# Performance work log

Measured on AMD Instinct MI355X. Metric: run time of the kernel, lower is better.

## Reference

```python
import jax, jax.numpy as jnp
import numpy as np

VOLUME_SIZE = 48  # max_disp / down = 192 / 4


def setup_inputs() -> dict:
    key = jax.random.key(0)
    k1, k2 = jax.random.split(key)
    b, c, h, w = 8, 128, 128, 240
    left_feature = jax.random.normal(k1, (b, c, h, w), dtype=jnp.float32)
    right_feature = jax.random.normal(k2, (b, c, h, w), dtype=jnp.float32)
    return {"left_feature": left_feature, "right_feature": right_feature}


def reference(left_feature, right_feature):
    # cost_volume[:, i, :, x] = mean_c(L[:, :, :, x] * R[:, :, :, x-i]) for x >= i, else 0
    b, c, h, w = left_feature.shape
    col = jnp.arange(w)

    def per_disp(i):
        # shift right feature right by i; zero out wrapped-around columns (< i)
        r_shift = jnp.roll(right_feature, i, axis=-1)  # [b,c,h,w]
        prod_mean = jnp.mean(left_feature * r_shift, axis=1)  # [b,h,w]
        return jnp.where(col >= i, prod_mean, 0.0)

    cv = jax.vmap(per_disp)(jnp.arange(VOLUME_SIZE))  # [V,b,h,w]
    return jnp.transpose(cv, (1, 0, 2, 3))  # [b,V,h,w]
```

## Files before the change

### kernel.cpp

```cpp
#include <hip/hip_runtime.h>

#define CV_B 8
#define CV_C 128
#define CV_H 128
#define CV_W 240
#define CV_V 48
#define LSTRIDE 136

typedef __attribute__((ext_vector_type(8))) short bf16x8;
typedef __attribute__((ext_vector_type(4))) float f32x4;

__device__ __forceinline__ unsigned int pack2_bf16(float f0, float f1) {
    unsigned int u0 = __float_as_uint(f0);
    unsigned int u1 = __float_as_uint(f1);
    u0 += 0x7fffu + ((u0 >> 16) & 1u);
    u1 += 0x7fffu + ((u1 >> 16) & 1u);
    return (u0 >> 16) | (u1 & 0xffff0000u);
}

__global__ __launch_bounds__(256, 4) void cost_volume_kernel(
        const float* __restrict__ Lf, const float* __restrict__ Rf,
        float* __restrict__ out)
{
    __shared__ __align__(16) short sL[16 * LSTRIDE];
    __shared__ __align__(16) short sR[64 * LSTRIDE];
    __shared__ float band[CV_V * 17];

    const int t   = threadIdx.x;
    const int xt  = blockIdx.x * 16;
    const int y   = blockIdx.y;
    const int b   = blockIdx.z;
    const int jt0 = xt - 48;

    const int plane = CV_H * CV_W;
    const float* Lbase = Lf + ((b * CV_C) * plane) + y * CV_W;
    const float* Rbase = Rf + ((b * CV_C) * plane) + y * CV_W;

    {
        const int xl = t & 15;
        const int c0 = (t >> 4) * 8;
        const float* p = Lbase + c0 * plane + (xt + xl);
        float v[8];
#pragma unroll
        for (int jj = 0; jj < 8; ++jj) v[jj] = p[jj * plane];
        uint4 w;
        w.x = pack2_bf16(v[0], v[1]);
        w.y = pack2_bf16(v[2], v[3]);
        w.z = pack2_bf16(v[4], v[5]);
        w.w = pack2_bf16(v[6], v[7]);
        *(uint4*)&sL[xl * LSTRIDE + c0] = w;
    }

    {
        const int jl = t & 63;
        const int cb = (t >> 6) * 32;
        const int jg = jt0 + jl;
        const bool ok = (jg >= 0);
        const float* p = Rbase + cb * plane + jg;
#pragma unroll
        for (int g = 0; g < 4; ++g) {
            float v[8];
#pragma unroll
            for (int jj = 0; jj < 8; ++jj)
                v[jj] = ok ? p[(g * 8 + jj) * plane] : 0.0f;
            uint4 w;
            w.x = pack2_bf16(v[0], v[1]);
            w.y = pack2_bf16(v[2], v[3]);
            w.z = pack2_bf16(v[4], v[5]);
            w.w = pack2_bf16(v[6], v[7]);
            *(uint4*)&sR[jl * LSTRIDE + cb + g * 8] = w;
        }
    }

    __syncthreads();

    const int lane = t & 63;
    const int wv   = t >> 6;
    const int n    = lane & 15;
    const int quad = lane >> 4;

    f32x4 acc = {0.f, 0.f, 0.f, 0.f};
#pragma unroll
    for (int ks = 0; ks < 4; ++ks) {
        const int k0 = ks * 32 + quad * 8;
        bf16x8 a  = *(const bf16x8*)&sL[n * LSTRIDE + k0];
        bf16x8 bb = *(const bf16x8*)&sR[(wv * 16 + n) * LSTRIDE + k0];
        acc = __builtin_amdgcn_mfma_f32_16x16x32_bf16(a, bb, acc, 0, 0, 0);
    }

    const int jg = jt0 + wv * 16 + n;
#pragma unroll
    for (int r = 0; r < 4; ++r) {
        const int xl = quad * 4 + r;
        const int i  = (xt + xl) - jg;
        if (i >= 0 && i < CV_V) band[i * 17 + xl] = acc[r] * (1.0f / 128.0f);
    }
    __syncthreads();

#pragma unroll
    for (int u = 0; u < 3; ++u) {
        const int idx = t + u * 256;
        const int i   = idx >> 4;
        const int xl  = idx & 15;
        out[((b * CV_V + i) * CV_H + y) * CV_W + xt + xl] = band[i * 17 + xl];
    }
}

extern "C" void kernel_launch(void* const* d_in, const int* in_sizes, int n_in,
                              void* d_out, int out_size, void* d_ws, size_t ws_size,
                              hipStream_t stream)
{
    const float* Lf = (const float*)d_in[0];
    const float* Rf = (const float*)d_in[1];
    float* o = (float*)d_out;
    dim3 grid(CV_W / 16, CV_H, CV_B);
    dim3 block(256);
    hipLaunchKernelGGL(cost_volume_kernel, grid, block, 0, stream, Lf, Rf, o);
}
```

Before: 304.2 us.

## Sweep whole image row per block with ring-buffered right-feature tiles and prefetch

Each block now processes one full image row, iterating over 15 column tiles instead of one tile per block. Right-feature tiles are kept in a 5-slot shared-memory ring, so each R column is loaded from global memory once rather than roughly four times. The next tile's loads are issued before the current tile's MFMA and store phase. The grid shrinks to 1024 blocks of 256 threads, which may lower occupancy and parallelism, and it adds two barriers per tile.

```diff
diff --git a/kernel.cpp b/kernel.cpp
--- a/kernel.cpp
+++ b/kernel.cpp
@@ -5,7 +5,9 @@
 #define CV_H 128
 #define CV_W 240
 #define CV_V 48
+#define NT   15
 #define LSTRIDE 136
+#define NSLOT 5
 
 typedef __attribute__((ext_vector_type(8))) short bf16x8;
 typedef __attribute__((ext_vector_type(4))) float f32x4;
@@ -22,56 +24,42 @@
         const float* __restrict__ Lf, const float* __restrict__ Rf,
         float* __restrict__ out)
 {
-    __shared__ __align__(16) short sL[16 * LSTRIDE];
-    __shared__ __align__(16) short sR[64 * LSTRIDE];
+    __shared__ __align__(16) short sL[2][16 * LSTRIDE];
+    __shared__ __align__(16) short sR[NSLOT][16 * LSTRIDE];
     __shared__ float band[CV_V * 17];
 
-    const int t   = threadIdx.x;
-    const int xt  = blockIdx.x * 16;
-    const int y   = blockIdx.y;
-    const int b   = blockIdx.z;
-    const int jt0 = xt - 48;
+    const int t = threadIdx.x;
+    const int y = blockIdx.x;
+    const int b = blockIdx.y;
 
     const int plane = CV_H * CV_W;
-    const float* Lbase = Lf + ((b * CV_C) * plane) + y * CV_W;
-    const float* Rbase = Rf + ((b * CV_C) * plane) + y * CV_W;
+    const float* Lrow = Lf + (b * CV_C) * plane + y * CV_W;
+    const float* Rrow = Rf + (b * CV_C) * plane + y * CV_W;
+
+    const int xl = t & 15;
+    const int c0 = (t >> 4) * 8;
 
     {
-        const int xl = t & 15;
-        const int c0 = (t >> 4) * 8;
-        const float* p = Lbase + c0 * plane + (xt + xl);
-        float v[8];
+        uint4 z = {0u, 0u, 0u, 0u};
+        short* base = &sR[2][0];
+        const int n128 = (3 * 16 * LSTRIDE) / 8;
+        for (int idx = t; idx < n128; idx += 256)
+            *(uint4*)&base[idx * 8] = z;
+    }
+    {
+        const float* pL = Lrow + c0 * plane + xl;
+        const float* pR = Rrow + c0 * plane + xl;
+        float lv[8], rv[8];
 #pragma unroll
-        for (int jj = 0; jj < 8; ++jj) v[jj] = p[jj * plane];
-        uint4 w;
-        w.x = pack2_bf16(v[0], v[1]);
-        w.y = pack2_bf16(v[2], v[3]);
-        w.z = pack2_bf16(v[4], v[5]);
-        w.w = pack2_bf16(v[6], v[7]);
-        *(uint4*)&sL[xl * LSTRIDE + c0] = w;
+        for (int jj = 0; jj < 8; ++jj) { lv[jj] = pL[jj * plane]; rv[jj] = pR[jj * plane]; }
+        uint4 wl, wr;
+        wl.x = pack2_bf16(lv[0], lv[1]); wl.y = pack2_bf16(lv[2], lv[3]);
+        wl.z = pack2_bf16(lv[4], lv[5]); wl.w = pack2_bf16(lv[6], lv[7]);
+        wr.x = pack2_bf16(rv[0], rv[1]); wr.y = pack2_bf16(rv[2], rv[3]);
+        wr.z = pack2_bf16(rv[4], rv[5]); wr.w = pack2_bf16(rv[6], rv[7]);
+        *(uint4*)&sL[0][xl * LSTRIDE + c0] = wl;
+        *(uint4*)&sR[0][xl * LSTRIDE + c0] = wr;
     }
-
-    {
-        const int jl = t & 63;
-        const int cb = (t >> 6) * 32;
-        const int jg = jt0 + jl;
-        const bool ok = (jg >= 0);
-        const float* p = Rbase + cb * plane + jg;
-#pragma unroll
-        for (int g = 0; g < 4; ++g) {
-            float v[8];
-#pragma unroll
-            for (int jj = 0; jj < 8; ++jj)
-                v[jj] = ok ? p[(g * 8 + jj) * plane] : 0.0f;
-            uint4 w;
-            w.x = pack2_bf16(v[0], v[1]);
-            w.y = pack2_bf16(v[2], v[3]);
-            w.z = pack2_bf16(v[4], v[5]);
-            w.w = pack2_bf16(v[6], v[7]);
-            *(uint4*)&sR[jl * LSTRIDE + cb + g * 8] = w;
-        }
-    }
-
     __syncthreads();
 
     const int lane = t & 63;
@@ -79,30 +67,57 @@
     const int n    = lane & 15;
     const int quad = lane >> 4;
 
-    f32x4 acc = {0.f, 0.f, 0.f, 0.f};
+    for (int tt = 0; tt < NT; ++tt) {
+        float lv[8], rv[8];
+        const bool pf = (tt + 1 < NT);
+        if (pf) {
+            const int xg = 16 * (tt + 1);
+            const float* pL = Lrow + c0 * plane + xg + xl;
+            const float* pR = Rrow + c0 * plane + xg + xl;
 #pragma unroll
-    for (int ks = 0; ks < 4; ++ks) {
-        const int k0 = ks * 32 + quad * 8;
-        bf16x8 a  = *(const bf16x8*)&sL[n * LSTRIDE + k0];
-        bf16x8 bb = *(const bf16x8*)&sR[(wv * 16 + n) * LSTRIDE + k0];
-        acc = __builtin_amdgcn_mfma_f32_16x16x32_bf16(a, bb, acc, 0, 0, 0);
-    }
+            for (int jj = 0; jj < 8; ++jj) { lv[jj] = pL[jj * plane]; rv[jj] = pR[jj * plane]; }
+        }
 
-    const int jg = jt0 + wv * 16 + n;
+        const int u    = tt - 3 + wv;
+        const int slot = (u + NSLOT) % NSLOT;
+        const short* aRow = &sL[tt & 1][n * LSTRIDE];
+        const short* bRow = &sR[slot][n * LSTRIDE];
+        f32x4 acc = {0.f, 0.f, 0.f, 0.f};
 #pragma unroll
-    for (int r = 0; r < 4; ++r) {
-        const int xl = quad * 4 + r;
-        const int i  = (xt + xl) - jg;
-        if (i >= 0 && i < CV_V) band[i * 17 + xl] = acc[r] * (1.0f / 128.0f);
-    }
-    __syncthreads();
+        for (int ks = 0; ks < 4; ++ks) {
+            const int k0 = ks * 32 + quad * 8;
+            bf16x8 a  = *(const bf16x8*)&aRow[k0];
+            bf16x8 bb = *(const bf16x8*)&bRow[k0];
+            acc = __builtin_amdgcn_mfma_f32_16x16x32_bf16(a, bb, acc, 0, 0, 0);
+        }
 
 #pragma unroll
-    for (int u = 0; u < 3; ++u) {
-        const int idx = t + u * 256;
-        const int i   = idx >> 4;
-        const int xl  = idx & 15;
-        out[((b * CV_V + i) * CV_H + y) * CV_W + xt + xl] = band[i * 17 + xl];
+        for (int r = 0; r < 4; ++r) {
+            const int xloc = quad * 4 + r;
+            const int i    = 16 * (3 - wv) + xloc - n;
+            if (i >= 0 && i < CV_V) band[i * 17 + xloc] = acc[r] * (1.0f / 128.0f);
+        }
+        __syncthreads();
+
+        const int xbase = 16 * tt;
+#pragma unroll
+        for (int uu = 0; uu < 3; ++uu) {
+            const int idx = t + uu * 256;
+            const int i   = idx >> 4;
+            const int xx  = idx & 15;
+            out[((b * CV_V + i) * CV_H + y) * CV_W + xbase + xx] = band[i * 17 + xx];
+        }
+
+        if (pf) {
+            uint4 wl, wr;
+            wl.x = pack2_bf16(lv[0], lv[1]); wl.y = pack2_bf16(lv[2], lv[3]);
+            wl.z = pack2_bf16(lv[4], lv[5]); wl.w = pack2_bf16(lv[6], lv[7]);
+            wr.x = pack2_bf16(rv[0], rv[1]); wr.y = pack2_bf16(rv[2], rv[3]);
+            wr.z = pack2_bf16(rv[4], rv[5]); wr.w = pack2_bf16(rv[6], rv[7]);
+            *(uint4*)&sL[(tt + 1) & 1][xl * LSTRIDE + c0] = wl;
+            *(uint4*)&sR[(tt + 1) % NSLOT][xl * LSTRIDE + c0] = wr;
+        }
+        __syncthreads();
     }
 }
 
@@ -113,7 +128,7 @@
     const float* Lf = (const float*)d_in[0];
     const float* Rf = (const float*)d_in[1];
     float* o = (float*)d_out;
-    dim3 grid(CV_W / 16, CV_H, CV_B);
+    dim3 grid(CV_H, CV_B);
     dim3 block(256);
     hipLaunchKernelGGL(cost_volume_kernel, grid, block, 0, stream, Lf, Rf, o);
 }
```

Result: faster. 294.6 us (-3.1%).

## Assign two x-tiles per wave and reuse right-feature fragments in registers

Applied to the files above, without the earlier changes.

Each wave now handles up to two 16-column output tiles and loads bf16 MFMA fragments straight from global memory into registers, so the shared-memory staging of L and R and the block-wide barriers go away. Right-feature windows are loaded once per wave and shared by both adjacent tiles, which cuts redundant R reads (previously 4x overlap per tile). The grid shrinks to 2 blocks per row, so there are fewer blocks and less parallelism. Global loads are now strided per lane rather than coalesced staging loads, which may hurt memory efficiency.

```diff
diff --git a/kernel.cpp b/kernel.cpp
--- a/kernel.cpp
+++ b/kernel.cpp
@@ -5,7 +5,7 @@
 #define CV_H 128
 #define CV_W 240
 #define CV_V 48
-#define LSTRIDE 136
+#define BSTRIDE 17
 
 typedef __attribute__((ext_vector_type(8))) short bf16x8;
 typedef __attribute__((ext_vector_type(4))) float f32x4;
@@ -18,91 +18,109 @@
     return (u0 >> 16) | (u1 & 0xffff0000u);
 }
 
+__device__ __forceinline__ bf16x8 pack8(const float v[8]) {
+    union { unsigned int u[4]; bf16x8 h; } cv;
+    cv.u[0] = pack2_bf16(v[0], v[1]);
+    cv.u[1] = pack2_bf16(v[2], v[3]);
+    cv.u[2] = pack2_bf16(v[4], v[5]);
+    cv.u[3] = pack2_bf16(v[6], v[7]);
+    return cv.h;
+}
+
 __global__ __launch_bounds__(256, 4) void cost_volume_kernel(
         const float* __restrict__ Lf, const float* __restrict__ Rf,
         float* __restrict__ out)
 {
-    __shared__ __align__(16) short sL[16 * LSTRIDE];
-    __shared__ __align__(16) short sR[64 * LSTRIDE];
-    __shared__ float band[CV_V * 17];
+    __shared__ float band[4][2][CV_V * BSTRIDE];
 
-    const int t   = threadIdx.x;
-    const int xt  = blockIdx.x * 16;
-    const int y   = blockIdx.y;
-    const int b   = blockIdx.z;
-    const int jt0 = xt - 48;
+    const int t    = threadIdx.x;
+    const int wv   = t >> 6;
+    const int lane = t & 63;
+    const int n    = lane & 15;
+    const int quad = lane >> 4;
+
+    const int half = blockIdx.x;
+    const int y    = blockIdx.y;
+    const int b    = blockIdx.z;
+
+    const int T0 = half * 8 + wv * 2;
+    const int nt = (T0 + 1 < 15) ? 2 : 1;
+    const int x0 = T0 * 16;
 
     const int plane = CV_H * CV_W;
-    const float* Lbase = Lf + ((b * CV_C) * plane) + y * CV_W;
-    const float* Rbase = Rf + ((b * CV_C) * plane) + y * CV_W;
+    const float* Lrow = Lf + (b * CV_C) * plane + y * CV_W;
+    const float* Rrow = Rf + (b * CV_C) * plane + y * CV_W;
 
-    {
-        const int xl = t & 15;
-        const int c0 = (t >> 4) * 8;
-        const float* p = Lbase + c0 * plane + (xt + xl);
-        float v[8];
+    const int kbase = quad * 8;
+
+    bf16x8 aF[2][4];
 #pragma unroll
-        for (int jj = 0; jj < 8; ++jj) v[jj] = p[jj * plane];
-        uint4 w;
-        w.x = pack2_bf16(v[0], v[1]);
-        w.y = pack2_bf16(v[2], v[3]);
-        w.z = pack2_bf16(v[4], v[5]);
-        w.w = pack2_bf16(v[6], v[7]);
-        *(uint4*)&sL[xl * LSTRIDE + c0] = w;
+    for (int e = 0; e < 2; ++e) {
+        if (e < nt) {
+            const float* p = Lrow + x0 + 16 * e + n;
+#pragma unroll
+            for (int ks = 0; ks < 4; ++ks) {
+                float v[8];
+#pragma unroll
+                for (int jj = 0; jj < 8; ++jj)
+                    v[jj] = p[(ks * 32 + kbase + jj) * plane];
+                aF[e][ks] = pack8(v);
+            }
+        }
     }
 
-    {
-        const int jl = t & 63;
-        const int cb = (t >> 6) * 32;
-        const int jg = jt0 + jl;
+    float* band0 = &band[wv][0][0];
+    float* band1 = &band[wv][1][0];
+
+    for (int w = T0 - 3; w <= T0 + nt - 1; ++w) {
+        const int j0 = 16 * w;
+        const int jg = j0 + n;
         const bool ok = (jg >= 0);
-        const float* p = Rbase + cb * plane + jg;
+        const float* p = Rrow + jg;
+
+        bf16x8 bF[4];
 #pragma unroll
-        for (int g = 0; g < 4; ++g) {
+        for (int ks = 0; ks < 4; ++ks) {
             float v[8];
 #pragma unroll
             for (int jj = 0; jj < 8; ++jj)
-                v[jj] = ok ? p[(g * 8 + jj) * plane] : 0.0f;
-            uint4 w;
-            w.x = pack2_bf16(v[0], v[1]);
-            w.y = pack2_bf16(v[2], v[3]);
-            w.z = pack2_bf16(v[4], v[5]);
-            w.w = pack2_bf16(v[6], v[7]);
-            *(uint4*)&sR[jl * LSTRIDE + cb + g * 8] = w;
+                v[jj] = ok ? p[(ks * 32 + kbase + jj) * plane] : 0.0f;
+            bF[ks] = pack8(v);
+        }
+
+#pragma unroll
+        for (int e = 0; e < 2; ++e) {
+            if (e < nt && w >= T0 + e - 3 && w <= T0 + e) {
+                f32x4 acc = {0.f, 0.f, 0.f, 0.f};
+#pragma unroll
+                for (int ks = 0; ks < 4; ++ks)
+                    acc = __builtin_amdgcn_mfma_f32_16x16x32_bf16(aF[e][ks], bF[ks], acc, 0, 0, 0);
+                float* bd = e ? band1 : band0;
+                const int ibase = 16 * (T0 + e - w);
+#pragma unroll
+                for (int r = 0; r < 4; ++r) {
+                    const int xloc = quad * 4 + r;
+                    const int i    = ibase + xloc - n;
+                    if (i >= 0 && i < CV_V)
+                        bd[i * BSTRIDE + xloc] = acc[r] * (1.0f / 128.0f);
+                }
+            }
         }
     }
 
-    __syncthreads();
-
-    const int lane = t & 63;
-    const int wv   = t >> 6;
-    const int n    = lane & 15;
-    const int quad = lane >> 4;
-
-    f32x4 acc = {0.f, 0.f, 0.f, 0.f};
 #pragma unroll
-    for (int ks = 0; ks < 4; ++ks) {
-        const int k0 = ks * 32 + quad * 8;
-        bf16x8 a  = *(const bf16x8*)&sL[n * LSTRIDE + k0];
-        bf16x8 bb = *(const bf16x8*)&sR[(wv * 16 + n) * LSTRIDE + k0];
-        acc = __builtin_amdgcn_mfma_f32_16x16x32_bf16(a, bb, acc, 0, 0, 0);
-    }
-
-    const int jg = jt0 + wv * 16 + n;
+    for (int e = 0; e < 2; ++e) {
+        if (e < nt) {
+            const float* bd = e ? band1 : band0;
+            const int xb = x0 + 16 * e;
 #pragma unroll
-    for (int r = 0; r < 4; ++r) {
-        const int xl = quad * 4 + r;
-        const int i  = (xt + xl) - jg;
-        if (i >= 0 && i < CV_V) band[i * 17 + xl] = acc[r] * (1.0f / 128.0f);
-    }
-    __syncthreads();
-
-#pragma unroll
-    for (int u = 0; u < 3; ++u) {
-        const int idx = t + u * 256;
-        const int i   = idx >> 4;
-        const int xl  = idx & 15;
-        out[((b * CV_V + i) * CV_H + y) * CV_W + xt + xl] = band[i * 17 + xl];
+            for (int uu = 0; uu < 12; ++uu) {
+                const int idx = lane + uu * 64;
+                const int i   = idx >> 4;
+                const int xx  = idx & 15;
+                out[((b * CV_V + i) * CV_H + y) * CV_W + xb + xx] = bd[i * BSTRIDE + xx];
+            }
+        }
     }
 }
 
@@ -113,7 +131,7 @@
     const float* Lf = (const float*)d_in[0];
     const float* Rf = (const float*)d_in[1];
     float* o = (float*)d_out;
-    dim3 grid(CV_W / 16, CV_H, CV_B);
+    dim3 grid(2, CV_H, CV_B);
     dim3 block(256);
     hipLaunchKernelGGL(cost_volume_kernel, grid, block, 0, stream, Lf, Rf, o);
 }
```

After: 305.4 us. No clear change (+0.4%).
